# Kernel optimization log

Hardware: AMD Instinct MI355X
Metric: run time of the kernel (lower is better)

The kernel has to match this reference:

```python
import jax, jax.numpy as jnp
import numpy as np

D_K = 128
SCALER = np.sqrt(D_K).astype(np.float32)

def setup_inputs() -> dict:
    key = jax.random.key(0)
    kq, kk, kv = jax.random.split(key, 3)
    B, L, D = 16, 2048, D_K
    q = jax.random.normal(kq, (B, L, D), dtype=jnp.float32)
    k = jax.random.normal(kk, (B, L, D), dtype=jnp.float32)
    v = jax.random.normal(kv, (B, L, D), dtype=jnp.float32)
    return {"q": q, "k": k, "v": v}

def reference(q, k, v):
    # score[b, i, j] = q[b, i, :] . k[b, j, :] / sqrt(d_k)
    score = jnp.einsum('bid,bjd->bij', q, k) / SCALER
    attn = jax.nn.softmax(score, axis=-1)
    # output[b, i, :] = sum_j attn[b, i, j] * v[b, j, :]
    return jnp.einsum('bij,bjd->bid', attn, v)
```

## Files before the change

### kernel.cpp

```cpp
#include <hip/hip_runtime.h>
#include <stdint.h>


typedef short bf16x8 __attribute__((ext_vector_type(8)));
typedef float f32x4 __attribute__((ext_vector_type(4)));
typedef unsigned int u32;
typedef unsigned short u16;

#define L_SEQ  2048
#define D_HEAD 128
#define TSZ    8388608u
#define W_PART (2u * TSZ)
#define W_LSUM (W_PART + 768u * 32768u)
#define WS_NEED (W_LSUM + 768u * 128u * 4u)

__device__ __forceinline__ unsigned pk2(float lo, float hi) {
    union { float f; unsigned u; } a, b;
    a.f = lo; b.f = hi;
    return __builtin_amdgcn_perm(b.u + 0x8000u, a.u + 0x8000u, 0x07060302u);
}
__device__ __forceinline__ float ex2(float x) { return __builtin_amdgcn_exp2f(x); }
__device__ __forceinline__ float bflo(unsigned w) {
    union { unsigned u; float f; } v; v.u = w << 16; return v.f;
}
__device__ __forceinline__ float bfhi(unsigned w) {
    union { unsigned u; float f; } v; v.u = w & 0xffff0000u; return v.f;
}
__device__ __forceinline__ void gl_lds16(const u16* g, u16* l) {
    __builtin_amdgcn_global_load_lds(
        (const __attribute__((address_space(1))) u32*)g,
        (__attribute__((address_space(3))) u32*)l, 16, 0, 0);
}

__global__ __launch_bounds__(256, 4)
void prepass(const float* __restrict__ K, const float* __restrict__ V,
             u16* __restrict__ kb, u16* __restrict__ vt) {
    const int id = blockIdx.x, t = threadIdx.x;
    if (id < 512) {
        const float* src = K + (size_t)id * 64 * 128;
        u16*        dst = kb + (size_t)id * 64 * 128;
        const int r = t >> 2;
        #pragma unroll
        for (int i = 0; i < 4; ++i) {
            int gp = (t & 3) * 4 + i;
            int gs = gp ^ (r & 7);
            const float* s = src + r * 128 + gs * 8;
            float4 x0 = *(const float4*)s, x1 = *(const float4*)(s + 4);
            uint4 w;
            w.x = pk2(x0.x, x0.y); w.y = pk2(x0.z, x0.w);
            w.z = pk2(x1.x, x1.y); w.w = pk2(x1.z, x1.w);
            *(uint4*)(dst + r * 128 + gp * 8) = w;
        }
    } else {
        __shared__ __align__(16) u16 vl[128 * 72];
        const int bid = id - 512;
        const float* src = V + (size_t)bid * 64 * 128;
        const int vcc = t & 31, vgk = t >> 5;
        union { float4 v; float f[4]; } vr[8];
        const float* vp = src + (size_t)(vgk * 8) * 128 + vcc * 4;
        #pragma unroll
        for (int r = 0; r < 8; ++r) vr[r].v = *(const float4*)(vp + (size_t)r * 128);
        #pragma unroll
        for (int dd = 0; dd < 4; ++dd) {
            uint4 w;
            w.x = pk2(vr[0].f[dd], vr[1].f[dd]);
            w.y = pk2(vr[2].f[dd], vr[3].f[dd]);
            w.z = pk2(vr[4].f[dd], vr[5].f[dd]);
            w.w = pk2(vr[6].f[dd], vr[7].f[dd]);
            *(uint4*)(&vl[(vcc * 4 + dd) * 72 + vgk * 8]) = w;
        }
        __syncthreads();
        u16* dst = vt + (size_t)bid * 8192;
        #pragma unroll
        for (int i = 0; i < 4; ++i) {
            int flat = t + 256 * i;
            int d = flat >> 3, gp = flat & 7;
            uint4 w = *(const uint4*)(&vl[d * 72 + ((gp ^ (d & 7)) * 8)]);
            *(uint4*)(dst + (size_t)flat * 8) = w;
        }
    }
}

__global__ __launch_bounds__(256, 2)
void attn3(const float* __restrict__ Qg, const u16* __restrict__ kb,
           const u16* __restrict__ vt, u16* __restrict__ part,
           float* __restrict__ lsum) {
    __shared__ __align__(16) char smem[49152];
    const int tid = threadIdx.x;
    const int wv = tid >> 6, lane = tid & 63;
    const int c = lane & 15, qd = lane >> 4, cx = c & 7;
    const int bid = blockIdx.x;
    const int p = bid & 255, kvh = bid >> 8;
    const int b = p & 15, qblk = p >> 4;
    const int t0 = kvh * 11;
    const int nt = (kvh < 2) ? 11 : 10;

    const float* Qp = Qg + (size_t)b * L_SEQ * D_HEAD;
    const u16*   Kp = kb + (size_t)b * L_SEQ * D_HEAD + (size_t)t0 * 8192;
    const u16*   Vp = vt + (size_t)b * 32 * 8192 + (size_t)t0 * 8192;
    u16* Kl = (u16*)smem;
    u16* Vl = (u16*)(smem + 16384);
    u16* Pl = (u16*)(smem + 32768) + wv * 2048;

    const int so = wv * 2048 + lane * 8;
    const int psw = (c & 7) << 1;

    #pragma unroll
    for (int i = 0; i < 4; ++i) {
        gl_lds16(Kp + so + i * 512, Kl + so + i * 512);
        gl_lds16(Vp + so + i * 512, Vl + so + i * 512);
    }

    const float QS = 1.4426950408889634f / 11.313708498984761f;
    bf16x8 qf[2][4];
    #pragma unroll
    for (int s = 0; s < 2; ++s) {
        const float* qrow = Qp + (size_t)(qblk * 128 + wv * 32 + s * 16 + c) * 128 + qd * 8;
        #pragma unroll
        for (int kt = 0; kt < 4; ++kt) {
            float4 x0 = *(const float4*)(qrow + kt * 32);
            float4 x1 = *(const float4*)(qrow + kt * 32 + 4);
            union { unsigned u[4]; bf16x8 v; } tt;
            tt.u[0] = pk2(x0.x * QS, x0.y * QS);
            tt.u[1] = pk2(x0.z * QS, x0.w * QS);
            tt.u[2] = pk2(x1.x * QS, x1.y * QS);
            tt.u[3] = pk2(x1.z * QS, x1.w * QS);
            qf[s][kt] = tt.v;
        }
    }

    f32x4 acc[2][8];
    #pragma unroll
    for (int s = 0; s < 2; ++s)
        #pragma unroll
        for (int dt = 0; dt < 8; ++dt) acc[s][dt] = (f32x4){0.f, 0.f, 0.f, 0.f};
    float lrun[2] = {0.f, 0.f};

    __syncthreads();

    for (int it = 0; it < nt; ++it) {
        f32x4 st[4][2];
        #pragma unroll
        for (int v = 0; v < 4; ++v) {
            st[v][0] = (f32x4){0.f, 0.f, 0.f, 0.f};
            st[v][1] = (f32x4){0.f, 0.f, 0.f, 0.f};
        }
        #pragma unroll
        for (int kt = 0; kt < 4; ++kt) {
            const int g = ((kt * 4 + qd) ^ cx) * 8;
            #pragma unroll
            for (int v = 0; v < 4; ++v) {
                bf16x8 a = *(const bf16x8*)(Kl + (v * 16 + c) * 128 + g);
                st[v][0] = __builtin_amdgcn_mfma_f32_16x16x32_bf16(a, qf[0][kt], st[v][0], 0, 0, 0);
                st[v][1] = __builtin_amdgcn_mfma_f32_16x16x32_bf16(a, qf[1][kt], st[v][1], 0, 0, 0);
            }
        }
        __syncthreads();

        if (it + 1 < nt) {
            const u16* kg = Kp + (size_t)(it + 1) * 8192 + so;
            #pragma unroll
            for (int i = 0; i < 4; ++i) gl_lds16(kg + i * 512, Kl + so + i * 512);
        }

        #pragma unroll
        for (int s = 0; s < 2; ++s) {
            float lsm = 0.f;
            #pragma unroll
            for (int v = 0; v < 4; ++v) {
                float p0 = ex2(st[v][s].x), p1 = ex2(st[v][s].y);
                float p2 = ex2(st[v][s].z), p3 = ex2(st[v][s].w);
                lsm += (p0 + p1) + (p2 + p3);
                uint2 w; w.x = pk2(p0, p1); w.y = pk2(p2, p3);
                int gsw = (v * 4 + qd) ^ psw;
                *(uint2*)(Pl + (s * 16 + c) * 64 + gsw * 4) = w;
            }
            lrun[s] += lsm;
        }
        bf16x8 pf[2][2];
        #pragma unroll
        for (int h = 0; h < 2; ++h) {
            int gsw = (h * 8 + qd * 2) ^ psw;
            #pragma unroll
            for (int s = 0; s < 2; ++s)
                pf[h][s] = *(const bf16x8*)(Pl + (s * 16 + c) * 64 + gsw * 4);
        }

        #pragma unroll
        for (int dt = 0; dt < 8; ++dt) {
            #pragma unroll
            for (int h = 0; h < 2; ++h) {
                bf16x8 a = *(const bf16x8*)(Vl + (dt * 16 + c) * 64 + ((h * 4 + qd) ^ cx) * 8);
                acc[0][dt] = __builtin_amdgcn_mfma_f32_16x16x32_bf16(a, pf[h][0], acc[0][dt], 0, 0, 0);
                acc[1][dt] = __builtin_amdgcn_mfma_f32_16x16x32_bf16(a, pf[h][1], acc[1][dt], 0, 0, 0);
            }
        }
        __syncthreads();

        if (it + 1 < nt) {
            const u16* vg = Vp + (size_t)(it + 1) * 8192 + so;
            #pragma unroll
            for (int i = 0; i < 4; ++i) gl_lds16(vg + i * 512, Vl + so + i * 512);
        }
    }

    float ls[2];
    #pragma unroll
    for (int s = 0; s < 2; ++s) {
        float l = lrun[s];
        l += __shfl_xor(l, 16);
        l += __shfl_xor(l, 32);
        ls[s] = l;
    }
    u16* pb = part + (size_t)bid * 16384;
    #pragma unroll
    for (int s = 0; s < 2; ++s)
        #pragma unroll
        for (int dt = 0; dt < 8; ++dt) {
            f32x4 o = acc[s][dt];
            uint2 w; w.x = pk2(o.x, o.y); w.y = pk2(o.z, o.w);
            *(uint2*)(pb + ((((wv * 2 + s) * 8 + dt) * 64 + lane) << 2)) = w;
        }
    if (qd == 0) {
        lsum[kvh * 32768 + p * 128 + wv * 32 + c]      = ls[0];
        lsum[kvh * 32768 + p * 128 + wv * 32 + 16 + c] = ls[1];
    }
}

__global__ __launch_bounds__(256, 2)
void combine3(const u16* __restrict__ part, const float* __restrict__ lsum,
              float* __restrict__ Og) {
    __shared__ float inv[128];
    __shared__ __align__(16) float Ol[64 * 132];
    const int t = threadIdx.x, p = blockIdx.x;
    const int b = p & 15, qblk = p >> 4;
    if (t < 128) {
        float l0 = lsum[p * 128 + t];
        float l1 = lsum[32768 + p * 128 + t];
        float l2 = lsum[65536 + p * 128 + t];
        inv[t] = 1.0f / (l0 + l1 + l2);
    }
    const uint2* P0 = (const uint2*)(part + (size_t)p * 16384);
    const uint2* P1 = (const uint2*)(part + (size_t)(256 + p) * 16384);
    const uint2* P2 = (const uint2*)(part + (size_t)(512 + p) * 16384);
    __syncthreads();
    #pragma unroll
    for (int h = 0; h < 2; ++h) {
        #pragma unroll
        for (int i = 0; i < 8; ++i) {
            int slot = i * 256 + t;
            int lc = slot >> 6, lane = slot & 63;
            int gc = h * 32 + lc;
            int s = (lc >> 3) & 1, dt = lc & 7;
            int qd = lane >> 4, c = lane & 15;
            int row = (lc >> 4) * 32 + s * 16 + c;
            int d0 = dt * 16 + qd * 4;
            size_t idx = (size_t)gc * 64 + lane;
            uint2 w0 = P0[idx], w1 = P1[idx], w2 = P2[idx];
            float iv = inv[h * 64 + row];
            float4 o;
            o.x = (bflo(w0.x) + bflo(w1.x) + bflo(w2.x)) * iv;
            o.y = (bfhi(w0.x) + bfhi(w1.x) + bfhi(w2.x)) * iv;
            o.z = (bflo(w0.y) + bflo(w1.y) + bflo(w2.y)) * iv;
            o.w = (bfhi(w0.y) + bfhi(w1.y) + bfhi(w2.y)) * iv;
            *(float4*)(&Ol[row * 132 + d0]) = o;
        }
        __syncthreads();
        #pragma unroll
        for (int i = 0; i < 8; ++i) {
            int slot = i * 256 + t;
            int row = slot >> 5, c4 = slot & 31;
            float4 val = *(const float4*)(&Ol[row * 132 + c4 * 4]);
            size_t q = (size_t)b * L_SEQ + qblk * 128 + h * 64 + row;
            *(float4*)(Og + q * D_HEAD + c4 * 4) = val;
        }
        __syncthreads();
    }
}

extern "C" void kernel_launch(void* const* d_in, const int* in_sizes, int n_in,
                              void* d_out, int out_size, void* d_ws, size_t ws_size,
                              hipStream_t stream) {
    const float* q = (const float*)d_in[0];
    const float* k = (const float*)d_in[1];
    const float* v = (const float*)d_in[2];
    float* out = (float*)d_out;
    u16* kb = (u16*)d_ws;
    u16* vt = (u16*)((char*)d_ws + TSZ);
    u16* part = (u16*)((char*)d_ws + W_PART);
    float* ls = (float*)((char*)d_ws + W_LSUM);
    prepass<<<dim3(1024), dim3(256), 0, stream>>>(k, v, kb, vt);
    attn3<<<dim3(768), dim3(256), 0, stream>>>(q, kb, vt, part, ls);
    combine3<<<dim3(256), dim3(256), 0, stream>>>(part, ls, out);
}
```

Measured before the change: 138.1 us.

## Double-buffer K/V in LDS and split the KV range in two

The attention kernel now holds two LDS buffers each for K and V. It prefetches the next tile at the top of each iteration, so it needs only one barrier per iteration instead of two. The KV range is split two ways (16 tiles per block) instead of three (11/11/10), which gives 512 blocks instead of 768 and removes a partial second wave and one partial-sum stream from the combine kernel. The per-wave P scratch is halved and reused for both row halves, with an explicit lgkmcnt wait between them. The costs are 72KB of LDS per block, a tighter occupancy budget, and more serial work per block.

New measurement: 137.6 us. No clear change (-0.4%).

```diff
diff --git a/kernel.cpp b/kernel.cpp
--- a/kernel.cpp
+++ b/kernel.cpp
@@ -82,33 +82,35 @@
 }
 
 __global__ __launch_bounds__(256, 2)
-void attn3(const float* __restrict__ Qg, const u16* __restrict__ kb,
+void attn2(const float* __restrict__ Qg, const u16* __restrict__ kb,
            const u16* __restrict__ vt, u16* __restrict__ part,
            float* __restrict__ lsum) {
-    __shared__ __align__(16) char smem[49152];
+    __shared__ __align__(16) char smem[73728];
     const int tid = threadIdx.x;
     const int wv = tid >> 6, lane = tid & 63;
     const int c = lane & 15, qd = lane >> 4, cx = c & 7;
     const int bid = blockIdx.x;
     const int p = bid & 255, kvh = bid >> 8;
     const int b = p & 15, qblk = p >> 4;
-    const int t0 = kvh * 11;
-    const int nt = (kvh < 2) ? 11 : 10;
+    const int t0 = kvh * 16;
+    const int nt = 16;
 
     const float* Qp = Qg + (size_t)b * L_SEQ * D_HEAD;
     const u16*   Kp = kb + (size_t)b * L_SEQ * D_HEAD + (size_t)t0 * 8192;
     const u16*   Vp = vt + (size_t)b * 32 * 8192 + (size_t)t0 * 8192;
-    u16* Kl = (u16*)smem;
-    u16* Vl = (u16*)(smem + 16384);
-    u16* Pl = (u16*)(smem + 32768) + wv * 2048;
+    u16* Pl = (u16*)(smem + 65536) + wv * 1024;
 
     const int so = wv * 2048 + lane * 8;
     const int psw = (c & 7) << 1;
 
-    #pragma unroll
-    for (int i = 0; i < 4; ++i) {
-        gl_lds16(Kp + so + i * 512, Kl + so + i * 512);
-        gl_lds16(Vp + so + i * 512, Vl + so + i * 512);
+    {
+        u16* K0 = (u16*)smem;
+        u16* V0 = (u16*)(smem + 32768);
+        #pragma unroll
+        for (int i = 0; i < 4; ++i) {
+            gl_lds16(Kp + so + i * 512, K0 + so + i * 512);
+            gl_lds16(Vp + so + i * 512, V0 + so + i * 512);
+        }
     }
 
     const float QS = 1.4426950408889634f / 11.313708498984761f;
@@ -138,7 +140,23 @@
 
     __syncthreads();
 
+    #pragma unroll 2
     for (int it = 0; it < nt; ++it) {
+        u16* Kc = (u16*)(smem + ((it & 1) << 14));
+        u16* Vc = (u16*)(smem + 32768 + ((it & 1) << 14));
+
+        if (it + 1 < nt) {
+            u16* Kn = (u16*)(smem + ((~it & 1) << 14));
+            u16* Vn = (u16*)(smem + 32768 + ((~it & 1) << 14));
+            const u16* kg = Kp + (size_t)(it + 1) * 8192 + so;
+            const u16* vg = Vp + (size_t)(it + 1) * 8192 + so;
+            #pragma unroll
+            for (int i = 0; i < 4; ++i) {
+                gl_lds16(kg + i * 512, Kn + so + i * 512);
+                gl_lds16(vg + i * 512, Vn + so + i * 512);
+            }
+        }
+
         f32x4 st[4][2];
         #pragma unroll
         for (int v = 0; v < 4; ++v) {
@@ -150,19 +168,13 @@
             const int g = ((kt * 4 + qd) ^ cx) * 8;
             #pragma unroll
             for (int v = 0; v < 4; ++v) {
-                bf16x8 a = *(const bf16x8*)(Kl + (v * 16 + c) * 128 + g);
+                bf16x8 a = *(const bf16x8*)(Kc + (v * 16 + c) * 128 + g);
                 st[v][0] = __builtin_amdgcn_mfma_f32_16x16x32_bf16(a, qf[0][kt], st[v][0], 0, 0, 0);
                 st[v][1] = __builtin_amdgcn_mfma_f32_16x16x32_bf16(a, qf[1][kt], st[v][1], 0, 0, 0);
             }
         }
-        __syncthreads();
-
-        if (it + 1 < nt) {
-            const u16* kg = Kp + (size_t)(it + 1) * 8192 + so;
-            #pragma unroll
-            for (int i = 0; i < 4; ++i) gl_lds16(kg + i * 512, Kl + so + i * 512);
-        }
-
+
+        bf16x8 pf[2][2];
         #pragma unroll
         for (int s = 0; s < 2; ++s) {
             float lsm = 0.f;
@@ -173,35 +185,28 @@
                 lsm += (p0 + p1) + (p2 + p3);
                 uint2 w; w.x = pk2(p0, p1); w.y = pk2(p2, p3);
                 int gsw = (v * 4 + qd) ^ psw;
-                *(uint2*)(Pl + (s * 16 + c) * 64 + gsw * 4) = w;
+                *(uint2*)(Pl + c * 64 + gsw * 4) = w;
             }
             lrun[s] += lsm;
-        }
-        bf16x8 pf[2][2];
-        #pragma unroll
-        for (int h = 0; h < 2; ++h) {
-            int gsw = (h * 8 + qd * 2) ^ psw;
-            #pragma unroll
-            for (int s = 0; s < 2; ++s)
-                pf[h][s] = *(const bf16x8*)(Pl + (s * 16 + c) * 64 + gsw * 4);
+            #pragma unroll
+            for (int h = 0; h < 2; ++h) {
+                int gsw = (h * 8 + qd * 2) ^ psw;
+                pf[h][s] = *(const bf16x8*)(Pl + c * 64 + gsw * 4);
+            }
+            if (s == 0) asm volatile("s_waitcnt lgkmcnt(0)" ::: "memory");
         }
 
         #pragma unroll
         for (int dt = 0; dt < 8; ++dt) {
             #pragma unroll
             for (int h = 0; h < 2; ++h) {
-                bf16x8 a = *(const bf16x8*)(Vl + (dt * 16 + c) * 64 + ((h * 4 + qd) ^ cx) * 8);
+                bf16x8 a = *(const bf16x8*)(Vc + (dt * 16 + c) * 64 + ((h * 4 + qd) ^ cx) * 8);
                 acc[0][dt] = __builtin_amdgcn_mfma_f32_16x16x32_bf16(a, pf[h][0], acc[0][dt], 0, 0, 0);
                 acc[1][dt] = __builtin_amdgcn_mfma_f32_16x16x32_bf16(a, pf[h][1], acc[1][dt], 0, 0, 0);
             }
         }
-        __syncthreads();
-
-        if (it + 1 < nt) {
-            const u16* vg = Vp + (size_t)(it + 1) * 8192 + so;
-            #pragma unroll
-            for (int i = 0; i < 4; ++i) gl_lds16(vg + i * 512, Vl + so + i * 512);
-        }
+
+        if (it + 1 < nt) __syncthreads();
     }
 
     float ls[2];
@@ -228,7 +233,7 @@
 }
 
 __global__ __launch_bounds__(256, 2)
-void combine3(const u16* __restrict__ part, const float* __restrict__ lsum,
+void combine2(const u16* __restrict__ part, const float* __restrict__ lsum,
               float* __restrict__ Og) {
     __shared__ float inv[128];
     __shared__ __align__(16) float Ol[64 * 132];
@@ -237,12 +242,10 @@
     if (t < 128) {
         float l0 = lsum[p * 128 + t];
         float l1 = lsum[32768 + p * 128 + t];
-        float l2 = lsum[65536 + p * 128 + t];
-        inv[t] = 1.0f / (l0 + l1 + l2);
+        inv[t] = 1.0f / (l0 + l1);
     }
     const uint2* P0 = (const uint2*)(part + (size_t)p * 16384);
     const uint2* P1 = (const uint2*)(part + (size_t)(256 + p) * 16384);
-    const uint2* P2 = (const uint2*)(part + (size_t)(512 + p) * 16384);
     __syncthreads();
     #pragma unroll
     for (int h = 0; h < 2; ++h) {
@@ -252,17 +255,17 @@
             int lc = slot >> 6, lane = slot & 63;
             int gc = h * 32 + lc;
             int s = (lc >> 3) & 1, dt = lc & 7;
-            int qd = lane >> 4, c = lane & 15;
-            int row = (lc >> 4) * 32 + s * 16 + c;
+            int qd = lane >> 4, cc = lane & 15;
+            int row = (lc >> 4) * 32 + s * 16 + cc;
             int d0 = dt * 16 + qd * 4;
             size_t idx = (size_t)gc * 64 + lane;
-            uint2 w0 = P0[idx], w1 = P1[idx], w2 = P2[idx];
+            uint2 w0 = P0[idx], w1 = P1[idx];
             float iv = inv[h * 64 + row];
             float4 o;
-            o.x = (bflo(w0.x) + bflo(w1.x) + bflo(w2.x)) * iv;
-            o.y = (bfhi(w0.x) + bfhi(w1.x) + bfhi(w2.x)) * iv;
-            o.z = (bflo(w0.y) + bflo(w1.y) + bflo(w2.y)) * iv;
-            o.w = (bfhi(w0.y) + bfhi(w1.y) + bfhi(w2.y)) * iv;
+            o.x = (bflo(w0.x) + bflo(w1.x)) * iv;
+            o.y = (bfhi(w0.x) + bfhi(w1.x)) * iv;
+            o.z = (bflo(w0.y) + bflo(w1.y)) * iv;
+            o.w = (bfhi(w0.y) + bfhi(w1.y)) * iv;
             *(float4*)(&Ol[row * 132 + d0]) = o;
         }
         __syncthreads();
@@ -290,6 +293,6 @@
     u16* part = (u16*)((char*)d_ws + W_PART);
     float* ls = (float*)((char*)d_ws + W_LSUM);
     prepass<<<dim3(1024), dim3(256), 0, stream>>>(k, v, kb, vt);
-    attn3<<<dim3(768), dim3(256), 0, stream>>>(q, kb, vt, part, ls);
-    combine3<<<dim3(256), dim3(256), 0, stream>>>(part, ls, out);
-}
+    attn2<<<dim3(512), dim3(256), 0, stream>>>(q, kb, vt, part, ls);
+    combine2<<<dim3(256), dim3(256), 0, stream>>>(part, ls, out);
+}
```

## Split attention tiles across 8 waves by key/d-half, reduce KV split to two

Applied to the files above, without the earlier changes.

Each attention block now runs 512 threads. Wave pairs share 32 query rows: each wave scores half of the 64-key tile and accumulates half of the output head dimension, exchanging probabilities through shared LDS. The KV sequence is split in two instead of three, so 512 blocks fit in a single wave of residency rather than a 768-block tail, and the combine kernel reads two partials instead of three. The cost is an extra barrier per tile for the shared P buffer, along with longer per-block loops.

Measured after the change: 136.6 us. No clear change (-1.1%).

```diff
diff --git a/kernel.cpp b/kernel.cpp
--- a/kernel.cpp
+++ b/kernel.cpp
@@ -11,8 +11,8 @@
 #define D_HEAD 128
 #define TSZ    8388608u
 #define W_PART (2u * TSZ)
-#define W_LSUM (W_PART + 768u * 32768u)
-#define WS_NEED (W_LSUM + 768u * 128u * 4u)
+#define W_LSUM (W_PART + 512u * 32768u)
+#define WS_NEED (W_LSUM + 512u * 256u * 4u)
 
 __device__ __forceinline__ unsigned pk2(float lo, float hi) {
     union { float f; unsigned u; } a, b;
@@ -81,41 +81,39 @@
     }
 }
 
-__global__ __launch_bounds__(256, 2)
-void attn3(const float* __restrict__ Qg, const u16* __restrict__ kb,
+__global__ __launch_bounds__(512, 4)
+void attnD(const float* __restrict__ Qg, const u16* __restrict__ kb,
            const u16* __restrict__ vt, u16* __restrict__ part,
            float* __restrict__ lsum) {
     __shared__ __align__(16) char smem[49152];
     const int tid = threadIdx.x;
     const int wv = tid >> 6, lane = tid & 63;
     const int c = lane & 15, qd = lane >> 4, cx = c & 7;
+    const int qs = wv >> 1, dh = wv & 1;
     const int bid = blockIdx.x;
-    const int p = bid & 255, kvh = bid >> 8;
+    const int kvh = bid >> 8, p = bid & 255;
     const int b = p & 15, qblk = p >> 4;
-    const int t0 = kvh * 11;
-    const int nt = (kvh < 2) ? 11 : 10;
+    const int nt = 16;
 
     const float* Qp = Qg + (size_t)b * L_SEQ * D_HEAD;
-    const u16*   Kp = kb + (size_t)b * L_SEQ * D_HEAD + (size_t)t0 * 8192;
-    const u16*   Vp = vt + (size_t)b * 32 * 8192 + (size_t)t0 * 8192;
+    const u16*   Kp = kb + (size_t)b * L_SEQ * D_HEAD + (size_t)kvh * 16 * 8192;
+    const u16*   Vp = vt + (size_t)b * 32 * 8192 + (size_t)kvh * 16 * 8192;
     u16* Kl = (u16*)smem;
     u16* Vl = (u16*)(smem + 16384);
-    u16* Pl = (u16*)(smem + 32768) + wv * 2048;
-
-    const int so = wv * 2048 + lane * 8;
-    const int psw = (c & 7) << 1;
-
-    #pragma unroll
-    for (int i = 0; i < 4; ++i) {
-        gl_lds16(Kp + so + i * 512, Kl + so + i * 512);
-        gl_lds16(Vp + so + i * 512, Vl + so + i * 512);
-    }
+    u16* Pq = (u16*)(smem + 32768) + qs * 2048;
+    const int psw = cx << 1;
+    const int so = tid * 8;
+
+    gl_lds16(Kp + so, Kl + so);
+    gl_lds16(Kp + so + 4096, Kl + so + 4096);
+    gl_lds16(Vp + so, Vl + so);
+    gl_lds16(Vp + so + 4096, Vl + so + 4096);
 
     const float QS = 1.4426950408889634f / 11.313708498984761f;
     bf16x8 qf[2][4];
     #pragma unroll
     for (int s = 0; s < 2; ++s) {
-        const float* qrow = Qp + (size_t)(qblk * 128 + wv * 32 + s * 16 + c) * 128 + qd * 8;
+        const float* qrow = Qp + (size_t)(qblk * 128 + qs * 32 + s * 16 + c) * 128 + qd * 8;
         #pragma unroll
         for (int kt = 0; kt < 4; ++kt) {
             float4 x0 = *(const float4*)(qrow + kt * 32);
@@ -129,19 +127,19 @@
         }
     }
 
-    f32x4 acc[2][8];
+    f32x4 acc[2][4];
     #pragma unroll
     for (int s = 0; s < 2; ++s)
         #pragma unroll
-        for (int dt = 0; dt < 8; ++dt) acc[s][dt] = (f32x4){0.f, 0.f, 0.f, 0.f};
+        for (int dt = 0; dt < 4; ++dt) acc[s][dt] = (f32x4){0.f, 0.f, 0.f, 0.f};
     float lrun[2] = {0.f, 0.f};
 
     __syncthreads();
 
     for (int it = 0; it < nt; ++it) {
-        f32x4 st[4][2];
-        #pragma unroll
-        for (int v = 0; v < 4; ++v) {
+        f32x4 st[2][2];
+        #pragma unroll
+        for (int v = 0; v < 2; ++v) {
             st[v][0] = (f32x4){0.f, 0.f, 0.f, 0.f};
             st[v][1] = (f32x4){0.f, 0.f, 0.f, 0.f};
         }
@@ -149,58 +147,59 @@
         for (int kt = 0; kt < 4; ++kt) {
             const int g = ((kt * 4 + qd) ^ cx) * 8;
             #pragma unroll
-            for (int v = 0; v < 4; ++v) {
-                bf16x8 a = *(const bf16x8*)(Kl + (v * 16 + c) * 128 + g);
+            for (int v = 0; v < 2; ++v) {
+                bf16x8 a = *(const bf16x8*)(Kl + (dh * 32 + v * 16 + c) * 128 + g);
                 st[v][0] = __builtin_amdgcn_mfma_f32_16x16x32_bf16(a, qf[0][kt], st[v][0], 0, 0, 0);
                 st[v][1] = __builtin_amdgcn_mfma_f32_16x16x32_bf16(a, qf[1][kt], st[v][1], 0, 0, 0);
             }
         }
-        __syncthreads();
-
-        if (it + 1 < nt) {
-            const u16* kg = Kp + (size_t)(it + 1) * 8192 + so;
-            #pragma unroll
-            for (int i = 0; i < 4; ++i) gl_lds16(kg + i * 512, Kl + so + i * 512);
-        }
 
         #pragma unroll
         for (int s = 0; s < 2; ++s) {
             float lsm = 0.f;
             #pragma unroll
-            for (int v = 0; v < 4; ++v) {
+            for (int v = 0; v < 2; ++v) {
                 float p0 = ex2(st[v][s].x), p1 = ex2(st[v][s].y);
                 float p2 = ex2(st[v][s].z), p3 = ex2(st[v][s].w);
                 lsm += (p0 + p1) + (p2 + p3);
                 uint2 w; w.x = pk2(p0, p1); w.y = pk2(p2, p3);
-                int gsw = (v * 4 + qd) ^ psw;
-                *(uint2*)(Pl + (s * 16 + c) * 64 + gsw * 4) = w;
+                int gsw = (dh * 8 + v * 4 + qd) ^ psw;
+                *(uint2*)(Pq + (s * 16 + c) * 64 + gsw * 4) = w;
             }
             lrun[s] += lsm;
         }
+        __syncthreads();
+
+        if (it + 1 < nt) {
+            const u16* kg = Kp + (size_t)(it + 1) * 8192 + so;
+            gl_lds16(kg, Kl + so);
+            gl_lds16(kg + 4096, Kl + so + 4096);
+        }
+
         bf16x8 pf[2][2];
         #pragma unroll
         for (int h = 0; h < 2; ++h) {
             int gsw = (h * 8 + qd * 2) ^ psw;
             #pragma unroll
             for (int s = 0; s < 2; ++s)
-                pf[h][s] = *(const bf16x8*)(Pl + (s * 16 + c) * 64 + gsw * 4);
-        }
-
-        #pragma unroll
-        for (int dt = 0; dt < 8; ++dt) {
+                pf[h][s] = *(const bf16x8*)(Pq + (s * 16 + c) * 64 + gsw * 4);
+        }
+        #pragma unroll
+        for (int dt = 0; dt < 4; ++dt) {
             #pragma unroll
             for (int h = 0; h < 2; ++h) {
-                bf16x8 a = *(const bf16x8*)(Vl + (dt * 16 + c) * 64 + ((h * 4 + qd) ^ cx) * 8);
-                acc[0][dt] = __builtin_amdgcn_mfma_f32_16x16x32_bf16(a, pf[h][0], acc[0][dt], 0, 0, 0);
-                acc[1][dt] = __builtin_amdgcn_mfma_f32_16x16x32_bf16(a, pf[h][1], acc[1][dt], 0, 0, 0);
+                bf16x8 av = *(const bf16x8*)(Vl + (dh * 64 + dt * 16 + c) * 64
+                                                + ((h * 4 + qd) ^ cx) * 8);
+                acc[0][dt] = __builtin_amdgcn_mfma_f32_16x16x32_bf16(av, pf[h][0], acc[0][dt], 0, 0, 0);
+                acc[1][dt] = __builtin_amdgcn_mfma_f32_16x16x32_bf16(av, pf[h][1], acc[1][dt], 0, 0, 0);
             }
         }
-        __syncthreads();
 
         if (it + 1 < nt) {
+            __syncthreads();
             const u16* vg = Vp + (size_t)(it + 1) * 8192 + so;
-            #pragma unroll
-            for (int i = 0; i < 4; ++i) gl_lds16(vg + i * 512, Vl + so + i * 512);
+            gl_lds16(vg, Vl + so);
+            gl_lds16(vg + 4096, Vl + so + 4096);
         }
     }
 
@@ -216,54 +215,59 @@
     #pragma unroll
     for (int s = 0; s < 2; ++s)
         #pragma unroll
-        for (int dt = 0; dt < 8; ++dt) {
+        for (int dt = 0; dt < 4; ++dt) {
             f32x4 o = acc[s][dt];
             uint2 w; w.x = pk2(o.x, o.y); w.y = pk2(o.z, o.w);
-            *(uint2*)(pb + ((((wv * 2 + s) * 8 + dt) * 64 + lane) << 2)) = w;
+            *(uint2*)(pb + ((((((qs * 2 + dh) * 2 + s) * 4 + dt) * 64) + lane) << 2)) = w;
         }
     if (qd == 0) {
-        lsum[kvh * 32768 + p * 128 + wv * 32 + c]      = ls[0];
-        lsum[kvh * 32768 + p * 128 + wv * 32 + 16 + c] = ls[1];
+        lsum[(size_t)bid * 256 + dh * 128 + qs * 32 + c]      = ls[0];
+        lsum[(size_t)bid * 256 + dh * 128 + qs * 32 + 16 + c] = ls[1];
     }
 }
 
 __global__ __launch_bounds__(256, 2)
-void combine3(const u16* __restrict__ part, const float* __restrict__ lsum,
+void combineD(const u16* __restrict__ part, const float* __restrict__ lsum,
               float* __restrict__ Og) {
     __shared__ float inv[128];
     __shared__ __align__(16) float Ol[64 * 132];
     const int t = threadIdx.x, p = blockIdx.x;
     const int b = p & 15, qblk = p >> 4;
     if (t < 128) {
-        float l0 = lsum[p * 128 + t];
-        float l1 = lsum[32768 + p * 128 + t];
-        float l2 = lsum[65536 + p * 128 + t];
-        inv[t] = 1.0f / (l0 + l1 + l2);
-    }
-    const uint2* P0 = (const uint2*)(part + (size_t)p * 16384);
-    const uint2* P1 = (const uint2*)(part + (size_t)(256 + p) * 16384);
-    const uint2* P2 = (const uint2*)(part + (size_t)(512 + p) * 16384);
+        float l = 0.f;
+        #pragma unroll
+        for (int kvh = 0; kvh < 2; ++kvh)
+            #pragma unroll
+            for (int dh = 0; dh < 2; ++dh)
+                l += lsum[(size_t)(kvh * 256 + p) * 256 + dh * 128 + t];
+        inv[t] = 1.0f / l;
+    }
+    const uint2* S0 = (const uint2*)(part + (size_t)p * 16384);
+    const uint2* S1 = (const uint2*)(part + (size_t)(256 + p) * 16384);
     __syncthreads();
     #pragma unroll
-    for (int h = 0; h < 2; ++h) {
+    for (int h2 = 0; h2 < 2; ++h2) {
         #pragma unroll
         for (int i = 0; i < 8; ++i) {
             int slot = i * 256 + t;
-            int lc = slot >> 6, lane = slot & 63;
-            int gc = h * 32 + lc;
-            int s = (lc >> 3) & 1, dt = lc & 7;
-            int qd = lane >> 4, c = lane & 15;
-            int row = (lc >> 4) * 32 + s * 16 + c;
-            int d0 = dt * 16 + qd * 4;
-            size_t idx = (size_t)gc * 64 + lane;
-            uint2 w0 = P0[idx], w1 = P1[idx], w2 = P2[idx];
-            float iv = inv[h * 64 + row];
+            int qs_l = slot >> 10;
+            int rem  = slot & 1023;
+            int dh = rem >> 9, s = (rem >> 8) & 1;
+            int dt = (rem >> 6) & 3, lane = rem & 63;
+            int qd = lane >> 4, cc = lane & 15;
+            int qs = h2 * 2 + qs_l;
+            int rowl = qs_l * 32 + s * 16 + cc;
+            int row  = h2 * 64 + rowl;
+            int d0 = dh * 64 + dt * 16 + qd * 4;
+            size_t idx = (size_t)((((qs * 2 + dh) * 2 + s) * 4 + dt) * 64 + lane);
+            uint2 w0 = S0[idx], w1 = S1[idx];
+            float iv = inv[row];
             float4 o;
-            o.x = (bflo(w0.x) + bflo(w1.x) + bflo(w2.x)) * iv;
-            o.y = (bfhi(w0.x) + bfhi(w1.x) + bfhi(w2.x)) * iv;
-            o.z = (bflo(w0.y) + bflo(w1.y) + bflo(w2.y)) * iv;
-            o.w = (bfhi(w0.y) + bfhi(w1.y) + bfhi(w2.y)) * iv;
-            *(float4*)(&Ol[row * 132 + d0]) = o;
+            o.x = (bflo(w0.x) + bflo(w1.x)) * iv;
+            o.y = (bfhi(w0.x) + bfhi(w1.x)) * iv;
+            o.z = (bflo(w0.y) + bflo(w1.y)) * iv;
+            o.w = (bfhi(w0.y) + bfhi(w1.y)) * iv;
+            *(float4*)(&Ol[rowl * 132 + d0]) = o;
         }
         __syncthreads();
         #pragma unroll
@@ -271,7 +275,7 @@
             int slot = i * 256 + t;
             int row = slot >> 5, c4 = slot & 31;
             float4 val = *(const float4*)(&Ol[row * 132 + c4 * 4]);
-            size_t q = (size_t)b * L_SEQ + qblk * 128 + h * 64 + row;
+            size_t q = (size_t)b * L_SEQ + qblk * 128 + h2 * 64 + row;
             *(float4*)(Og + q * D_HEAD + c4 * 4) = val;
         }
         __syncthreads();
@@ -290,6 +294,6 @@
     u16* part = (u16*)((char*)d_ws + W_PART);
     float* ls = (float*)((char*)d_ws + W_LSUM);
     prepass<<<dim3(1024), dim3(256), 0, stream>>>(k, v, kb, vt);
-    attn3<<<dim3(768), dim3(256), 0, stream>>>(q, kb, vt, part, ls);
-    combine3<<<dim3(256), dim3(256), 0, stream>>>(part, ls, out);
-}
+    attnD<<<dim3(512), dim3(512), 0, stream>>>(q, kb, vt, part, ls);
+    combineD<<<dim3(256), dim3(256), 0, stream>>>(part, ls, out);
+}
```
